# Optimization experiments

Measured on AMD Instinct MI355X. Metric: run time of the kernel, lower is better.

## Reference

```python
import jax, jax.numpy as jnp
import numpy as np

TEMPERATURE = 0.2
EPS = 1e-12  # F.normalize clamp eps


def setup_inputs() -> dict:
    key = jax.random.key(0)
    k1, k2 = jax.random.split(key)
    N, D = 4096, 256
    Z_1 = jax.random.normal(k1, (N, D), dtype=jnp.float32)
    Z_2 = jax.random.normal(k2, (N, D), dtype=jnp.float32)
    return {"Z_1": Z_1, "Z_2": Z_2}


def reference(Z_1, Z_2):
    N = Z_1.shape[0]
    M = 2 * N
    # concat views and L2-normalize rows (torch F.normalize semantics)
    Z = jnp.concatenate([Z_1, Z_2], axis=0)  # [2N, D]
    Z = Z / jnp.maximum(jnp.linalg.norm(Z, axis=1, keepdims=True), EPS)
    # full similarity matrix [2N, 2N]
    sim = jnp.matmul(Z, Z.T) / TEMPERATURE
    # positive for row i is column (i + N) mod 2N (other view of same sample,
    # identity diagonal discarded as in create_contrastive_masks)
    idx = jnp.arange(M)
    pos = sim[idx, (idx + N) % M]  # [2N]
    # logits = [pos, negatives]; label = 0 => CE = logsumexp(pos U negs) - pos.
    # pos U negs = all columns except the identity diagonal.
    diag = idx[:, None] == idx[None, :]
    sim_masked = jnp.where(diag, -jnp.inf, sim)
    lse = jax.nn.logsumexp(sim_masked, axis=1)  # [2N]
    return jnp.mean(lse - pos)
```

## Files before the change

kernel.cpp:

```cpp
#include <hip/hip_runtime.h>
#include <cstdint>
#include <cstddef>

#define TINV 5.0f
#define C5L2E 7.2134752044448170f
#define NROWS 4096
#define DDIM 256
#define MM 8192

typedef __bf16 bf16x8 __attribute__((ext_vector_type(8)));
typedef int i32x4 __attribute__((ext_vector_type(4)));
typedef float f32x4 __attribute__((ext_vector_type(4)));

typedef const void __attribute__((address_space(1)))* gas_ptr;
typedef void __attribute__((address_space(3)))* las_ptr;

__global__ __launch_bounds__(256, 2)
void nrm_kernel(const float* __restrict__ Z1, const float* __restrict__ Z2,
                unsigned short* __restrict__ Zb, float* __restrict__ rowsumAcc) {
    if (blockIdx.x < 32) rowsumAcc[blockIdx.x * 256 + threadIdx.x] = 0.f;
    const int w = threadIdx.x >> 6, lane = threadIdx.x & 63;
    const int row = blockIdx.x * 4 + w;
    const float* src = row < NROWS ? Z1 + (size_t)row * DDIM
                                   : Z2 + (size_t)(row - NROWS) * DDIM;
    float4 v = reinterpret_cast<const float4*>(src)[lane];
    float ss = v.x*v.x + v.y*v.y + v.z*v.z + v.w*v.w;
    #pragma unroll
    for (int m = 1; m < 64; m <<= 1) ss += __shfl_xor(ss, m, 64);
    float inv = 1.0f / fmaxf(sqrtf(ss), 1e-12f);
    float o[4] = { v.x*inv, v.y*inv, v.z*inv, v.w*inv };
    unsigned short us[4];
    #pragma unroll
    for (int e = 0; e < 4; ++e) {
        unsigned int b = __builtin_bit_cast(unsigned int, o[e]);
        b += 0x7FFFu + ((b >> 16) & 1u);
        us[e] = (unsigned short)(b >> 16);
    }
    reinterpret_cast<ushort4*>(Zb + (size_t)row * DDIM)[lane] =
        *reinterpret_cast<ushort4*>(us);
}

__device__ __forceinline__ void stage32(const unsigned short* Zb, char* ldsdst,
                                        int rowStart, int tid) {
    const char* base = reinterpret_cast<const char*>(Zb) + (size_t)rowStart * 512;
    #pragma unroll
    for (int it = 0; it < 4; ++it) {
        int L = it * 8192 + tid * 16;
        int row = L >> 9;
        int soff = row * 512 + ((L & 511) ^ ((row & 15) << 4));
        __builtin_amdgcn_global_load_lds((gas_ptr)(base + soff), (las_ptr)(ldsdst + L),
                                         16, 0, 0);
    }
}

__global__ __launch_bounds__(512, 2)
void sim_lse_kernel(const unsigned short* __restrict__ Zb,
                    float* __restrict__ rowsumAcc,
                    float* __restrict__ posArr) {
    __shared__ char lds[65536];
    __shared__ float colRed[4][64];
    const int tid = threadIdx.x;
    const int lane = tid & 63;
    const int w = tid >> 6;
    const int wr = w >> 1, wc = w & 1;
    const int r15 = lane & 15, hi = lane >> 4;
    const int r = blockIdx.x >> 3;
    const int s = blockIdx.x & 7;
    const int R0 = r * 256;
    const int nt = (s < 4) ? 9 : 8;

    auto colOf = [&](int t) -> int {
        int d, q;
        if (t == 8)        { d = 16;                  q = s; }
        else if (s == 7)   { if (t < 4) { d = 8; q = t; } else { d = 0; q = t - 4; } }
        else               { d = (t < 4) ? s + 1 : s + 9; q = t & 3; }
        return ((r + d) & 31) * 256 + q * 64;
    };

    stage32(Zb, lds, colOf(0), tid);

    i32x4 qf[4][8];
    {
        const char* abase = reinterpret_cast<const char*>(Zb)
                          + (size_t)(R0 + wr * 64 + r15) * 512 + hi * 16;
        #pragma unroll
        for (int mf = 0; mf < 4; ++mf)
            #pragma unroll
            for (int kk = 0; kk < 8; ++kk)
                qf[mf][kk] = *reinterpret_cast<const i32x4*>(abase + mf * 8192 + kk * 64);
    }

    int baddr0[8];
    #pragma unroll
    for (int kk = 0; kk < 8; ++kk)
        baddr0[kk] = (wc * 32 + r15) * 512 + (((hi << 4) | (kk << 6)) ^ (r15 << 4));

    float rowsum[4][4] = {{0,0,0,0},{0,0,0,0},{0,0,0,0},{0,0,0,0}};
    const int iBase = R0 + wr * 64 + (hi << 2);

    for (int t = 0; t < nt; ++t) {
        const int C0 = colOf(t);
        const int cur = (t & 1) << 15;
        if (t < nt - 1) {
            stage32(Zb, lds + (cur ^ 32768), colOf(t + 1), tid);
            asm volatile("s_waitcnt vmcnt(4)" ::: "memory");
        } else {
            asm volatile("s_waitcnt vmcnt(0)" ::: "memory");
        }
        __builtin_amdgcn_s_barrier();
        __builtin_amdgcn_sched_barrier(0);

        const int mode = (t == 8) ? 2 : ((s == 7 && t >= 4) ? 1 : 0);
        #pragma unroll
        for (int nf = 0; nf < 2; ++nf) {
            f32x4 acc[4] = {{0,0,0,0},{0,0,0,0},{0,0,0,0},{0,0,0,0}};
            #pragma unroll
            for (int kk = 0; kk < 8; ++kk) {
                i32x4 b = *reinterpret_cast<const i32x4*>(lds + cur + nf * 8192 + baddr0[kk]);
                #pragma unroll
                for (int mf = 0; mf < 4; ++mf)
                    asm("v_mfma_f32_16x16x32_bf16 %0, %1, %2, %0"
                        : "+v"(acc[mf]) : "a"(qf[mf][kk]), "v"(b));
            }
            const int j = C0 + wc * 32 + nf * 16 + r15;
            if (mode == 0) {
                float s8 = 0.f;
                #pragma unroll
                for (int mf = 0; mf < 4; ++mf)
                    #pragma unroll
                    for (int rr = 0; rr < 4; ++rr) {
                        float e = __builtin_amdgcn_exp2f(fmaf(acc[mf][rr], C5L2E, -C5L2E));
                        rowsum[mf][rr] += e;
                        s8 += e;
                    }
                s8 += __shfl_xor(s8, 16, 64);
                s8 += __shfl_xor(s8, 32, 64);
                if (hi == 0) colRed[wr][wc * 32 + nf * 16 + r15] = s8;
            } else if (mode == 1) {
                #pragma unroll
                for (int mf = 0; mf < 4; ++mf)
                    #pragma unroll
                    for (int rr = 0; rr < 4; ++rr) {
                        const int i = iBase + mf * 16 + rr;
                        if (j != i)
                            rowsum[mf][rr] += __builtin_amdgcn_exp2f(fmaf(acc[mf][rr], C5L2E, -C5L2E));
                    }
            } else {
                #pragma unroll
                for (int mf = 0; mf < 4; ++mf)
                    #pragma unroll
                    for (int rr = 0; rr < 4; ++rr) {
                        const int i = iBase + mf * 16 + rr;
                        rowsum[mf][rr] += __builtin_amdgcn_exp2f(fmaf(acc[mf][rr], C5L2E, -C5L2E));
                        if (j == (i ^ 4096)) posArr[i] = acc[mf][rr] * TINV;
                    }
            }
        }
        asm volatile("s_waitcnt lgkmcnt(0)" ::: "memory");
        __builtin_amdgcn_sched_barrier(0);
        __builtin_amdgcn_s_barrier();

        if (mode == 0 && tid < 64) {
            float v = colRed[0][tid] + colRed[1][tid] + colRed[2][tid] + colRed[3][tid];
            atomicAdd(&rowsumAcc[C0 + tid], v);
        }
    }

    #pragma unroll
    for (int mf = 0; mf < 4; ++mf)
        #pragma unroll
        for (int rr = 0; rr < 4; ++rr) {
            float v = rowsum[mf][rr];
            v += __shfl_xor(v, 1, 64);
            v += __shfl_xor(v, 2, 64);
            v += __shfl_xor(v, 4, 64);
            v += __shfl_xor(v, 8, 64);
            if (r15 == 0) atomicAdd(&rowsumAcc[iBase + mf * 16 + rr], v);
        }
}

__global__ __launch_bounds__(128)
void fin1_kernel(const float* __restrict__ rowsumAcc, const float* __restrict__ posArr,
                 float* __restrict__ blockSums) {
    const int tid = threadIdx.x;
    const int i = blockIdx.x * 128 + tid;
    double v = (double)(logf(rowsumAcc[i]) + 5.0f - posArr[i]);
    #pragma unroll
    for (int m = 1; m < 64; m <<= 1) v += __shfl_xor(v, m, 64);
    __shared__ double red[2];
    if ((tid & 63) == 0) red[tid >> 6] = v;
    __syncthreads();
    if (tid == 0) blockSums[blockIdx.x] = (float)(red[0] + red[1]);
}

__global__ __launch_bounds__(64)
void fin2_kernel(const float* __restrict__ blockSums, float* __restrict__ out) {
    double v = (double)blockSums[threadIdx.x];
    #pragma unroll
    for (int m = 1; m < 64; m <<= 1) v += __shfl_xor(v, m, 64);
    if (threadIdx.x == 0) out[0] = (float)(v / (double)MM);
}

extern "C" void kernel_launch(void* const* d_in, const int* in_sizes, int n_in,
                              void* d_out, int out_size, void* d_ws, size_t ws_size,
                              hipStream_t stream) {
    const float* Z1 = (const float*)d_in[0];
    const float* Z2 = (const float*)d_in[1];
    float* out = (float*)d_out;
    char* ws = (char*)d_ws;
    unsigned short* Zb = (unsigned short*)ws;
    float* posArr = (float*)(ws + (size_t)MM * DDIM * 2);
    float* rowsumAcc = (float*)(ws + (size_t)MM * DDIM * 2 + MM * 4);
    float* blockSums = (float*)(ws + (size_t)MM * DDIM * 2 + 2 * MM * 4);

    nrm_kernel<<<MM / 4, 256, 0, stream>>>(Z1, Z2, Zb, rowsumAcc);
    sim_lse_kernel<<<32 * 8, 512, 0, stream>>>(Zb, rowsumAcc, posArr);
    fin1_kernel<<<64, 128, 0, stream>>>(rowsumAcc, posArr, blockSums);
    fin2_kernel<<<1, 64, 0, stream>>>(blockSums, out);
}
```

Baseline: 46.28 us.

## Halve row tiles to 128 and replace atomics with partial-sum buffers

The similarity kernel now uses 128-row tiles with 256-thread blocks, and the launch grows to 512 blocks over a 64-tile symmetric schedule with its own diagonal and positive-pair handling. Atomic accumulation into a shared row-sum array is replaced by deterministic per-block partial row and column sums written to separate buffers. The finalize kernel then reduces 78 partials per row. This removes atomics, the LDS column reduction and one barrier wait, and raises parallelism. The cost is more global writes and reads in the finalize step, plus more B-tile staging per row.

```diff
diff --git a/kernel.cpp b/kernel.cpp
--- a/kernel.cpp
+++ b/kernel.cpp
@@ -17,8 +17,7 @@
 
 __global__ __launch_bounds__(256, 2)
 void nrm_kernel(const float* __restrict__ Z1, const float* __restrict__ Z2,
-                unsigned short* __restrict__ Zb, float* __restrict__ rowsumAcc) {
-    if (blockIdx.x < 32) rowsumAcc[blockIdx.x * 256 + threadIdx.x] = 0.f;
+                unsigned short* __restrict__ Zb) {
     const int w = threadIdx.x >> 6, lane = threadIdx.x & 63;
     const int row = blockIdx.x * 4 + w;
     const float* src = row < NROWS ? Z1 + (size_t)row * DDIM
@@ -44,8 +43,8 @@
                                         int rowStart, int tid) {
     const char* base = reinterpret_cast<const char*>(Zb) + (size_t)rowStart * 512;
     #pragma unroll
-    for (int it = 0; it < 4; ++it) {
-        int L = it * 8192 + tid * 16;
+    for (int it = 0; it < 8; ++it) {
+        int L = it * 4096 + tid * 16;
         int row = L >> 9;
         int soff = row * 512 + ((L & 511) ^ ((row & 15) << 4));
         __builtin_amdgcn_global_load_lds((gas_ptr)(base + soff), (las_ptr)(ldsdst + L),
@@ -53,12 +52,12 @@
     }
 }
 
-__global__ __launch_bounds__(512, 2)
+__global__ __launch_bounds__(256, 2)
 void sim_lse_kernel(const unsigned short* __restrict__ Zb,
-                    float* __restrict__ rowsumAcc,
+                    float* __restrict__ rowPart,
+                    float* __restrict__ colPartT,
                     float* __restrict__ posArr) {
     __shared__ char lds[65536];
-    __shared__ float colRed[4][64];
     const int tid = threadIdx.x;
     const int lane = tid & 63;
     const int w = tid >> 6;
@@ -66,15 +65,15 @@
     const int r15 = lane & 15, hi = lane >> 4;
     const int r = blockIdx.x >> 3;
     const int s = blockIdx.x & 7;
-    const int R0 = r * 256;
-    const int nt = (s < 4) ? 9 : 8;
+    const int R0 = r * 128;
+    const int e0 = r & 7, e1 = e0 ^ 4;
+    const int nt = 8 + ((s == e0) || (s == e1));
+    const int extraHalf = (s == e1) ? 1 : 0;
 
     auto colOf = [&](int t) -> int {
-        int d, q;
-        if (t == 8)        { d = 16;                  q = s; }
-        else if (s == 7)   { if (t < 4) { d = 8; q = t; } else { d = 0; q = t - 4; } }
-        else               { d = (t < 4) ? s + 1 : s + 9; q = t & 3; }
-        return ((r + d) & 31) * 256 + q * 64;
+        if (t == 8) return ((r + 32) & 63) * 128 + extraHalf * 64;
+        int d = s + ((t >> 1) << 3);
+        return ((r + d) & 63) * 128 + (t & 1) * 64;
     };
 
     stage32(Zb, lds, colOf(0), tid);
@@ -90,10 +89,10 @@
                 qf[mf][kk] = *reinterpret_cast<const i32x4*>(abase + mf * 8192 + kk * 64);
     }
 
-    int baddr0[8];
+    int baddr[8];
     #pragma unroll
     for (int kk = 0; kk < 8; ++kk)
-        baddr0[kk] = (wc * 32 + r15) * 512 + (((hi << 4) | (kk << 6)) ^ (r15 << 4));
+        baddr[kk] = (wc * 32 + r15) * 512 + (((hi << 4) | (kk << 6)) ^ (r15 << 4));
 
     float rowsum[4][4] = {{0,0,0,0},{0,0,0,0},{0,0,0,0},{0,0,0,0}};
     const int iBase = R0 + wr * 64 + (hi << 2);
@@ -103,20 +102,21 @@
         const int cur = (t & 1) << 15;
         if (t < nt - 1) {
             stage32(Zb, lds + (cur ^ 32768), colOf(t + 1), tid);
-            asm volatile("s_waitcnt vmcnt(4)" ::: "memory");
+            asm volatile("s_waitcnt vmcnt(8)" ::: "memory");
         } else {
             asm volatile("s_waitcnt vmcnt(0)" ::: "memory");
         }
         __builtin_amdgcn_s_barrier();
         __builtin_amdgcn_sched_barrier(0);
 
-        const int mode = (t == 8) ? 2 : ((s == 7 && t >= 4) ? 1 : 0);
+        const int mode = (t == 8) ? 2 : ((s == 0 && t < 2) ? 1 : 0);
+        const int d = s + ((t >> 1) << 3);
         #pragma unroll
         for (int nf = 0; nf < 2; ++nf) {
             f32x4 acc[4] = {{0,0,0,0},{0,0,0,0},{0,0,0,0},{0,0,0,0}};
             #pragma unroll
             for (int kk = 0; kk < 8; ++kk) {
-                i32x4 b = *reinterpret_cast<const i32x4*>(lds + cur + nf * 8192 + baddr0[kk]);
+                i32x4 b = *reinterpret_cast<const i32x4*>(lds + cur + nf * 8192 + baddr[kk]);
                 #pragma unroll
                 for (int mf = 0; mf < 4; ++mf)
                     asm("v_mfma_f32_16x16x32_bf16 %0, %1, %2, %0"
@@ -135,7 +135,8 @@
                     }
                 s8 += __shfl_xor(s8, 16, 64);
                 s8 += __shfl_xor(s8, 32, 64);
-                if (hi == 0) colRed[wr][wc * 32 + nf * 16 + r15] = s8;
+                if (hi == 0)
+                    colPartT[(size_t)(((d - 1) << 1) | wr) * MM + j] = s8;
             } else if (mode == 1) {
                 #pragma unroll
                 for (int mf = 0; mf < 4; ++mf)
@@ -156,14 +157,9 @@
                     }
             }
         }
-        asm volatile("s_waitcnt lgkmcnt(0)" ::: "memory");
+        asm volatile("" ::: "memory");
         __builtin_amdgcn_sched_barrier(0);
         __builtin_amdgcn_s_barrier();
-
-        if (mode == 0 && tid < 64) {
-            float v = colRed[0][tid] + colRed[1][tid] + colRed[2][tid] + colRed[3][tid];
-            atomicAdd(&rowsumAcc[C0 + tid], v);
-        }
     }
 
     #pragma unroll
@@ -175,16 +171,22 @@
             v += __shfl_xor(v, 2, 64);
             v += __shfl_xor(v, 4, 64);
             v += __shfl_xor(v, 8, 64);
-            if (r15 == 0) atomicAdd(&rowsumAcc[iBase + mf * 16 + rr], v);
+            if (r15 == 0)
+                rowPart[(size_t)((s << 1) | wc) * MM + iBase + mf * 16 + rr] = v;
         }
 }
 
 __global__ __launch_bounds__(128)
-void fin1_kernel(const float* __restrict__ rowsumAcc, const float* __restrict__ posArr,
-                 float* __restrict__ blockSums) {
+void fin1_kernel(const float* __restrict__ rowPart, const float* __restrict__ colPartT,
+                 const float* __restrict__ posArr, float* __restrict__ blockSums) {
     const int tid = threadIdx.x;
     const int i = blockIdx.x * 128 + tid;
-    double v = (double)(logf(rowsumAcc[i]) + 5.0f - posArr[i]);
+    float se = 0.f;
+    #pragma unroll
+    for (int p = 0; p < 16; ++p) se += rowPart[(size_t)p * MM + i];
+    #pragma unroll
+    for (int q = 0; q < 62; ++q) se += colPartT[(size_t)q * MM + i];
+    double v = (double)(logf(se) + 5.0f - posArr[i]);
     #pragma unroll
     for (int m = 1; m < 64; m <<= 1) v += __shfl_xor(v, m, 64);
     __shared__ double red[2];
@@ -209,12 +211,13 @@
     float* out = (float*)d_out;
     char* ws = (char*)d_ws;
     unsigned short* Zb = (unsigned short*)ws;
-    float* posArr = (float*)(ws + (size_t)MM * DDIM * 2);
-    float* rowsumAcc = (float*)(ws + (size_t)MM * DDIM * 2 + MM * 4);
-    float* blockSums = (float*)(ws + (size_t)MM * DDIM * 2 + 2 * MM * 4);
-
-    nrm_kernel<<<MM / 4, 256, 0, stream>>>(Z1, Z2, Zb, rowsumAcc);
-    sim_lse_kernel<<<32 * 8, 512, 0, stream>>>(Zb, rowsumAcc, posArr);
-    fin1_kernel<<<64, 128, 0, stream>>>(rowsumAcc, posArr, blockSums);
+    float* posArr   = (float*)(ws + 4194304);
+    float* rowPart  = (float*)(ws + 4194304 + 32768);
+    float* colPartT = (float*)(ws + 4194304 + 32768 + 524288);
+    float* blockSums= (float*)(ws + 4194304 + 32768 + 524288 + 2031616);
+
+    nrm_kernel<<<MM / 4, 256, 0, stream>>>(Z1, Z2, Zb);
+    sim_lse_kernel<<<64 * 8, 256, 0, stream>>>(Zb, rowPart, colPartT, posArr);
+    fin1_kernel<<<64, 128, 0, stream>>>(rowPart, colPartT, posArr, blockSums);
     fin2_kernel<<<1, 64, 0, stream>>>(blockSums, out);
 }
```

Result: slower. 66.06 us (+42.7%).
